# Performance work log

Hardware: AMD Instinct MI355X
Metric: run time of the kernel (lower is better)

## Reference

```python
import jax, jax.numpy as jnp
import numpy as np

N = 100000   # num_nodes
R = 8        # num_relations
D = 64       # hidden_dim
E = 3200000  # num_edges


def setup_inputs() -> dict:
    key = jax.random.key(0)
    ks = jax.random.split(key, 10)
    s = 1.0 / np.sqrt(D)
    return {
        "x": jnp.arange(N, dtype=jnp.int64),
        "edge_index": jax.random.randint(ks[0], (2, E), 0, N, dtype=jnp.int64),
        "edge_type": jax.random.randint(ks[1], (E,), 0, R, dtype=jnp.int64),
        "emb": jax.random.normal(ks[2], (N, D), dtype=jnp.float32),
        "W1": jax.random.normal(ks[3], (R, D, D), dtype=jnp.float32) * s,
        "root1": jax.random.normal(ks[4], (D, D), dtype=jnp.float32) * s,
        "b1": jnp.zeros((D,), dtype=jnp.float32),
        "W2": jax.random.normal(ks[5], (R, D, D), dtype=jnp.float32) * s,
        "root2": jax.random.normal(ks[6], (D, D), dtype=jnp.float32) * s,
        "b2": jnp.zeros((D,), dtype=jnp.float32),
    }


def rgcn_conv(h, W, root, b, src, dst, etype):
    # per-edge gather of source features: [E, D]
    msgs = h[src]
    # composite segment id: (dst, relation) -> dst * R + relation
    seg = dst * R + etype
    sums = jax.ops.segment_sum(msgs, seg, num_segments=N * R)          # [N*R, D]
    cnt = jax.ops.segment_sum(jnp.ones((msgs.shape[0],), h.dtype), seg,
                              num_segments=N * R)                       # [N*R]
    mean = sums / jnp.maximum(cnt, 1.0)[:, None]                        # per-relation mean aggr
    mean = mean.reshape(N, R, D)
    # relation-specific transform + root weight + bias
    return jnp.einsum('nrd,rde->ne', mean, W) + h @ root + b


def reference(x, edge_index, edge_type, emb, W1, root1, b1, W2, root2, b2):
    src, dst = edge_index[0], edge_index[1]
    h = emb[x]                                   # embedding lookup
    h = rgcn_conv(h, W1, root1, b1, src, dst, edge_type)
    h = jax.nn.relu(h)                           # dropout = identity (eval mode)
    h = rgcn_conv(h, W2, root2, b2, src, dst, edge_type)
    return h
```

## Files before the change

kernel.cpp:

```cpp
#include <hip/hip_runtime.h>

#define N_NODES 100000
#define R_REL   8
#define D_DIM   64
#define E_EDGES 3200000
#define NSEG    (N_NODES * R_REL)
#define NB      782
#define SEG_PER_BKT 1024
#define BKT_CAP 4800
#define P1_BLOCKS 625
#define P1_CHUNK  5120

typedef __attribute__((ext_vector_type(8))) short short8;
typedef __attribute__((ext_vector_type(4))) float f32x4;

__device__ __forceinline__ unsigned short f2bf(float f) {
    unsigned u = __float_as_uint(f);
    u += 0x7fffu + ((u >> 16) & 1u);
    return (unsigned short)(u >> 16);
}

__device__ __forceinline__ int epack(int s, int d, int r) {
    return (s << 10) | ((d & 127) << 3) | r;
}

__global__ void __launch_bounds__(256)
cvt_kernel(const float* __restrict__ in, unsigned short* __restrict__ outb) {
    size_t base = ((size_t)blockIdx.x * 256 + threadIdx.x) * 8;
    float4 v0 = *(const float4*)(in + base);
    float4 v1 = *(const float4*)(in + base + 4);
    uint4 o;
    o.x = f2bf(v0.x) | ((unsigned)f2bf(v0.y) << 16);
    o.y = f2bf(v0.z) | ((unsigned)f2bf(v0.w) << 16);
    o.z = f2bf(v1.x) | ((unsigned)f2bf(v1.y) << 16);
    o.w = f2bf(v1.z) | ((unsigned)f2bf(v1.w) << 16);
    *(uint4*)(outb + base) = o;
}

__global__ void init_cursor_kernel(int* __restrict__ bkt_cursor) {
    int t = blockIdx.x * 256 + threadIdx.x;
    if (t <= NB) bkt_cursor[t] = t * BKT_CAP;
}

__global__ void __launch_bounds__(256)
p1_scatter_kernel(const int* __restrict__ src, const int* __restrict__ dst,
                  const int* __restrict__ et, int* __restrict__ bkt_cursor,
                  int* __restrict__ packed) {
    __shared__ int hist[NB];
    __shared__ int cur[NB];
    int t = threadIdx.x;
    for (int i = t; i < NB; i += 256) hist[i] = 0;
    __syncthreads();
    int base = blockIdx.x * P1_CHUNK;
    for (int i = t * 4; i < P1_CHUNK; i += 1024) {
        int4 d4 = *(const int4*)(dst + base + i);
        atomicAdd(&hist[d4.x >> 7], 1);
        atomicAdd(&hist[d4.y >> 7], 1);
        atomicAdd(&hist[d4.z >> 7], 1);
        atomicAdd(&hist[d4.w >> 7], 1);
    }
    __syncthreads();
    for (int i = t; i < NB; i += 256) {
        int c = hist[i];
        cur[i] = c ? atomicAdd(&bkt_cursor[i], c) : 0;
    }
    __syncthreads();
    for (int i = t * 4; i < P1_CHUNK; i += 1024) {
        int4 s4 = *(const int4*)(src + base + i);
        int4 d4 = *(const int4*)(dst + base + i);
        int4 t4 = *(const int4*)(et  + base + i);
        int p0 = atomicAdd(&cur[d4.x >> 7], 1); packed[p0] = epack(s4.x, d4.x, t4.x);
        int p1 = atomicAdd(&cur[d4.y >> 7], 1); packed[p1] = epack(s4.y, d4.y, t4.y);
        int p2 = atomicAdd(&cur[d4.z >> 7], 1); packed[p2] = epack(s4.z, d4.z, t4.z);
        int p3 = atomicAdd(&cur[d4.w >> 7], 1); packed[p3] = epack(s4.w, d4.w, t4.w);
    }
}

__global__ void __launch_bounds__(256)
p2_sort_kernel(const int* __restrict__ packed, const int* __restrict__ bkt_cursor,
               int* __restrict__ starts, int* __restrict__ ends, int* __restrict__ esrc) {
    __shared__ int spk[BKT_CAP];
    __shared__ int shist[SEG_PER_BKT];
    __shared__ int scur[SEG_PER_BKT];
    __shared__ int stmp[256];
    int b = blockIdx.x;
    int t = threadIdx.x;
    int ebase = b * BKT_CAP;
    int ecnt  = bkt_cursor[b] - ebase;
    int segbase = b * SEG_PER_BKT;
    int nseg = NSEG - segbase; if (nseg > SEG_PER_BKT) nseg = SEG_PER_BKT;
#pragma unroll
    for (int i = 0; i < 4; ++i) shist[t + i * 256] = 0;
    __syncthreads();
    for (int i = t; i < ecnt; i += 256) {
        int p = packed[ebase + i];
        spk[i] = p;
        atomicAdd(&shist[p & 1023], 1);
    }
    __syncthreads();
    int loc[4], s = 0;
    int b4 = t * 4;
#pragma unroll
    for (int i = 0; i < 4; ++i) { loc[i] = shist[b4 + i]; s += loc[i]; }
    stmp[t] = s;
    __syncthreads();
    for (int off = 1; off < 256; off <<= 1) {
        int x = (t >= off) ? stmp[t - off] : 0;
        __syncthreads();
        stmp[t] += x;
        __syncthreads();
    }
    int run = (t == 0) ? 0 : stmp[t - 1];
#pragma unroll
    for (int i = 0; i < 4; ++i) {
        shist[b4 + i] = run; scur[b4 + i] = run;
        run += loc[i];
    }
    __syncthreads();
    for (int i = t; i < nseg; i += 256)
        starts[segbase + i] = ebase + shist[i];
    for (int i = t; i < ecnt; i += 256) {
        int p = spk[i];
        int r = atomicAdd(&scur[p & 1023], 1);
        esrc[ebase + r] = p >> 10;
    }
    __syncthreads();
    for (int i = t; i < nseg; i += 256)
        ends[segbase + i] = ebase + scur[i];
}

__global__ void wprep_kernel(const float* __restrict__ W, const float* __restrict__ root,
                             unsigned short* __restrict__ wbuf) {
    int r = blockIdx.x;
    const float* src = (r < 8) ? (W + (size_t)r * 4096) : root;
    __shared__ float t[64][65];
    int a = threadIdx.x >> 2, c = threadIdx.x & 3;
#pragma unroll
    for (int i = 0; i < 4; ++i) {
        float4 v = *(const float4*)(src + a * 64 + c * 16 + i * 4);
        t[a][c * 16 + i * 4 + 0] = v.x;
        t[a][c * 16 + i * 4 + 1] = v.y;
        t[a][c * 16 + i * 4 + 2] = v.z;
        t[a][c * 16 + i * 4 + 3] = v.w;
    }
    __syncthreads();
    unsigned short* outrow = wbuf + (size_t)r * 4096 + a * 64;
#pragma unroll
    for (int i = 0; i < 4; ++i) {
        int k0 = c * 16 + i * 4;
        ushort4 o;
        o.x = f2bf(t[k0 + 0][a]); o.y = f2bf(t[k0 + 1][a]);
        o.z = f2bf(t[k0 + 2][a]); o.w = f2bf(t[k0 + 3][a]);
        *(ushort4*)(outrow + k0) = o;
    }
}

__global__ void __launch_bounds__(512, 6)
fused_kernel(const unsigned short* __restrict__ hb, const int* __restrict__ esrc,
             const int* __restrict__ starts, const int* __restrict__ ends,
             const unsigned short* __restrict__ wbuf, const float* __restrict__ bias,
             void* __restrict__ out, int mode) {
    __shared__ unsigned short As[8][32][72];
    __shared__ int sS[256], sE[256];
    __shared__ int pool;
    int tid = threadIdx.x;
    int ml  = tid & 15;
    int n0  = blockIdx.x * 32;
    int sblk = n0 * R_REL;

    if (tid < 256) sS[tid] = starts[sblk + tid];
    else           sE[tid - 256] = ends[sblk + tid - 256];
    if (tid == 0) pool = 0;
    __syncthreads();

#define ACC4(P0,P1,P2,P3, RW, M)                                         \
    do {                                                                 \
        _Pragma("unroll")                                                \
        for (int i = 0; i < 4; ++i) if (i < (M)) {                       \
            P0 += __uint_as_float(RW[i].x << 16);                        \
            P1 += __uint_as_float(RW[i].x & 0xffff0000u);                \
            P2 += __uint_as_float(RW[i].y << 16);                        \
            P3 += __uint_as_float(RW[i].y & 0xffff0000u);                \
        }                                                                \
    } while (0)

#define LOAD4(RW, B, E)                                                  \
    do {                                                                 \
        _Pragma("unroll")                                                \
        for (int i = 0; i < 4; ++i) {                                    \
            int ee = (B) + i; ee = (ee < (E)) ? ee : ((E) - 1);          \
            int sid = esrc[ee];                                          \
            RW[i] = *(const uint2*)(hb + (size_t)sid * D_DIM + ml * 4);  \
        }                                                                \
    } while (0)

    while (true) {
        int s2 = 0;
        if (ml == 0) s2 = atomicAdd(&pool, 2);
        s2 = __shfl(s2, 0, 16);
        if (s2 >= 256) break;
        int b0 = sS[s2],     e0 = sE[s2];
        int b1 = sS[s2 + 1], e1 = sE[s2 + 1];
        int c0 = e0 - b0, c1 = e1 - b1;
        float p0 = 0.f, p1 = 0.f, p2 = 0.f, p3 = 0.f;
        float q0 = 0.f, q1 = 0.f, q2 = 0.f, q3 = 0.f;
        while (b0 < e0 || b1 < e1) {
            int m0 = e0 - b0; m0 = (m0 > 4) ? 4 : m0;
            int m1 = e1 - b1; m1 = (m1 > 4) ? 4 : m1;
            uint2 rA[4], rB[4];
            if (m0 > 0) LOAD4(rA, b0, e0);
            if (m1 > 0) LOAD4(rB, b1, e1);
            if (m0 > 0) { ACC4(p0, p1, p2, p3, rA, m0); b0 += m0; }
            if (m1 > 0) { ACC4(q0, q1, q2, q3, rB, m1); b1 += m1; }
        }
        int nl = s2 >> 3, r = s2 & 7;
        {
            float inv = __builtin_amdgcn_rcpf(fmaxf((float)c0, 1.0f));
            ushort4 o;
            o.x = f2bf(p0 * inv); o.y = f2bf(p1 * inv);
            o.z = f2bf(p2 * inv); o.w = f2bf(p3 * inv);
            *(ushort4*)(&As[r][nl][ml * 4]) = o;
        }
        {
            float inv = __builtin_amdgcn_rcpf(fmaxf((float)c1, 1.0f));
            ushort4 o;
            o.x = f2bf(q0 * inv); o.y = f2bf(q1 * inv);
            o.z = f2bf(q2 * inv); o.w = f2bf(q3 * inv);
            *(ushort4*)(&As[r + 1][nl][ml * 4]) = o;
        }
    }
#undef ACC4
#undef LOAD4

    int w  = tid >> 6;
    int kg = (tid >> 4) & 3;
    int h  = w & 1;
    int q  = w >> 1;

    const unsigned short* rp = hb + (size_t)(n0 + h * 16 + ml) * D_DIM + kg * 8;
    short8 RA0 = *(const short8*)(rp);
    short8 RA1 = *(const short8*)(rp + 32);

    __syncthreads();

    f32x4 acc = {0, 0, 0, 0};
#pragma unroll 1
    for (int p = 0; p < 8; ++p) {
        short8 A0 = *(const short8*)(&As[p][h * 16 + ml][kg * 8]);
        short8 A1 = *(const short8*)(&As[p][h * 16 + ml][kg * 8 + 32]);
        const unsigned short* bp = wbuf + (size_t)p * 4096 + (q * 16 + ml) * 64 + kg * 8;
        short8 B0 = *(const short8*)(bp);
        short8 B1 = *(const short8*)(bp + 32);
        acc = __builtin_amdgcn_mfma_f32_16x16x32_bf16(A0, B0, acc, 0, 0, 0);
        acc = __builtin_amdgcn_mfma_f32_16x16x32_bf16(A1, B1, acc, 0, 0, 0);
    }
    {
        const unsigned short* bp = wbuf + (size_t)8 * 4096 + (q * 16 + ml) * 64 + kg * 8;
        short8 B0 = *(const short8*)(bp);
        short8 B1 = *(const short8*)(bp + 32);
        acc = __builtin_amdgcn_mfma_f32_16x16x32_bf16(RA0, B0, acc, 0, 0, 0);
        acc = __builtin_amdgcn_mfma_f32_16x16x32_bf16(RA1, B1, acc, 0, 0, 0);
    }

    float bv = bias[q * 16 + ml];
#pragma unroll
    for (int rg = 0; rg < 4; ++rg) {
        int node = n0 + h * 16 + kg * 4 + rg;
        float v = acc[rg] + bv;
        if (mode) {
            v = fmaxf(v, 0.f);
            ((unsigned short*)out)[(size_t)node * D_DIM + q * 16 + ml] = f2bf(v);
        } else {
            ((float*)out)[(size_t)node * D_DIM + q * 16 + ml] = v;
        }
    }
}


extern "C" void kernel_launch(void* const* d_in, const int* in_sizes, int n_in,
                              void* d_out, int out_size, void* d_ws, size_t ws_size,
                              hipStream_t stream) {
    const int*   ei    = (const int*)d_in[1];
    const int*   src   = ei;
    const int*   dst   = ei + E_EDGES;
    const int*   et    = (const int*)d_in[2];
    const float* emb   = (const float*)d_in[3];
    const float* W1    = (const float*)d_in[4];
    const float* root1 = (const float*)d_in[5];
    const float* b1    = (const float*)d_in[6];
    const float* W2    = (const float*)d_in[7];
    const float* root2 = (const float*)d_in[8];
    const float* b2    = (const float*)d_in[9];
    float*       out   = (float*)d_out;

    unsigned short* embb   = (unsigned short*)d_ws;
    unsigned short* h1b    = embb + (size_t)N_NODES * D_DIM;
    unsigned short* wbuf1  = h1b + (size_t)N_NODES * D_DIM;
    unsigned short* wbuf2  = wbuf1 + 9 * 4096;
    int*            starts = (int*)(wbuf2 + 9 * 4096);
    int*            ends   = starts + NSEG;
    int*            packed = ends + NSEG;
    int*            esrc   = packed + (size_t)NB * BKT_CAP;
    int*            bkt_cursor = esrc + (size_t)NB * BKT_CAP;

    init_cursor_kernel<<<4, 256, 0, stream>>>(bkt_cursor);
    p1_scatter_kernel <<<P1_BLOCKS, 256, 0, stream>>>(src, dst, et, bkt_cursor, packed);
    p2_sort_kernel    <<<NB, 256, 0, stream>>>(packed, bkt_cursor, starts, ends, esrc);

    wprep_kernel<<<9, 256, 0, stream>>>(W1, root1, wbuf1);
    wprep_kernel<<<9, 256, 0, stream>>>(W2, root2, wbuf2);
    cvt_kernel<<<(N_NODES * D_DIM) / 2048, 256, 0, stream>>>(emb, embb);

    const int blocks = N_NODES / 32;

    fused_kernel<<<blocks, 512, 0, stream>>>(embb, esrc, starts, ends, wbuf1, b1, h1b, 1);
    fused_kernel<<<blocks, 512, 0, stream>>>(h1b, esrc, starts, ends, wbuf2, b2, out, 0);
}
```

Baseline: 459.8 us.

## Balance edge aggregation across waves by edge ranges and merge prep kernels

The aggregation phase of the fused kernel now stages the block's source-index list in LDS and splits the block's edge range evenly across the 8 waves. Each wave walks consecutive segments, with one lane per feature reading 2-byte values. Segments that cross a wave boundary are merged through shared-memory atomics in a fix-up pass. This replaces dynamic per-segment assignment and is meant to remove load imbalance from varying segment sizes. It adds LDS staging, a zeroing pass, an extra barrier, and smaller per-lane loads, and it assumes at most 1536 edges per block. The two weight-prep launches and the embedding conversion are also combined into a single kernel.

```diff
diff --git a/kernel.cpp b/kernel.cpp
--- a/kernel.cpp
+++ b/kernel.cpp
@@ -10,6 +10,7 @@
 #define BKT_CAP 4800
 #define P1_BLOCKS 625
 #define P1_CHUNK  5120
+#define ESRC_CAP 1536
 
 typedef __attribute__((ext_vector_type(8))) short short8;
 typedef __attribute__((ext_vector_type(4))) float f32x4;
@@ -22,19 +23,6 @@
 
 __device__ __forceinline__ int epack(int s, int d, int r) {
     return (s << 10) | ((d & 127) << 3) | r;
-}
-
-__global__ void __launch_bounds__(256)
-cvt_kernel(const float* __restrict__ in, unsigned short* __restrict__ outb) {
-    size_t base = ((size_t)blockIdx.x * 256 + threadIdx.x) * 8;
-    float4 v0 = *(const float4*)(in + base);
-    float4 v1 = *(const float4*)(in + base + 4);
-    uint4 o;
-    o.x = f2bf(v0.x) | ((unsigned)f2bf(v0.y) << 16);
-    o.y = f2bf(v0.z) | ((unsigned)f2bf(v0.w) << 16);
-    o.z = f2bf(v1.x) | ((unsigned)f2bf(v1.y) << 16);
-    o.w = f2bf(v1.z) | ((unsigned)f2bf(v1.w) << 16);
-    *(uint4*)(outb + base) = o;
 }
 
 __global__ void init_cursor_kernel(int* __restrict__ bkt_cursor) {
@@ -129,29 +117,49 @@
         ends[segbase + i] = ebase + scur[i];
 }
 
-__global__ void wprep_kernel(const float* __restrict__ W, const float* __restrict__ root,
-                             unsigned short* __restrict__ wbuf) {
-    int r = blockIdx.x;
-    const float* src = (r < 8) ? (W + (size_t)r * 4096) : root;
-    __shared__ float t[64][65];
-    int a = threadIdx.x >> 2, c = threadIdx.x & 3;
-#pragma unroll
-    for (int i = 0; i < 4; ++i) {
-        float4 v = *(const float4*)(src + a * 64 + c * 16 + i * 4);
-        t[a][c * 16 + i * 4 + 0] = v.x;
-        t[a][c * 16 + i * 4 + 1] = v.y;
-        t[a][c * 16 + i * 4 + 2] = v.z;
-        t[a][c * 16 + i * 4 + 3] = v.w;
-    }
-    __syncthreads();
-    unsigned short* outrow = wbuf + (size_t)r * 4096 + a * 64;
-#pragma unroll
-    for (int i = 0; i < 4; ++i) {
-        int k0 = c * 16 + i * 4;
-        ushort4 o;
-        o.x = f2bf(t[k0 + 0][a]); o.y = f2bf(t[k0 + 1][a]);
-        o.z = f2bf(t[k0 + 2][a]); o.w = f2bf(t[k0 + 3][a]);
-        *(ushort4*)(outrow + k0) = o;
+__global__ void __launch_bounds__(256)
+prep_kernel(const float* __restrict__ W1, const float* __restrict__ root1,
+            const float* __restrict__ W2, const float* __restrict__ root2,
+            const float* __restrict__ emb,
+            unsigned short* __restrict__ wbuf1, unsigned short* __restrict__ wbuf2,
+            unsigned short* __restrict__ embb) {
+    int b = blockIdx.x;
+    if (b < 18) {
+        int r = (b < 9) ? b : b - 9;
+        const float* W    = (b < 9) ? W1 : W2;
+        const float* root = (b < 9) ? root1 : root2;
+        unsigned short* wbuf = (b < 9) ? wbuf1 : wbuf2;
+        const float* src = (r < 8) ? (W + (size_t)r * 4096) : root;
+        __shared__ float t[64][65];
+        int a = threadIdx.x >> 2, c = threadIdx.x & 3;
+#pragma unroll
+        for (int i = 0; i < 4; ++i) {
+            float4 v = *(const float4*)(src + a * 64 + c * 16 + i * 4);
+            t[a][c * 16 + i * 4 + 0] = v.x;
+            t[a][c * 16 + i * 4 + 1] = v.y;
+            t[a][c * 16 + i * 4 + 2] = v.z;
+            t[a][c * 16 + i * 4 + 3] = v.w;
+        }
+        __syncthreads();
+        unsigned short* outrow = wbuf + (size_t)r * 4096 + a * 64;
+#pragma unroll
+        for (int i = 0; i < 4; ++i) {
+            int k0 = c * 16 + i * 4;
+            ushort4 o;
+            o.x = f2bf(t[k0 + 0][a]); o.y = f2bf(t[k0 + 1][a]);
+            o.z = f2bf(t[k0 + 2][a]); o.w = f2bf(t[k0 + 3][a]);
+            *(ushort4*)(outrow + k0) = o;
+        }
+    } else {
+        size_t base = ((size_t)(b - 18) * 256 + threadIdx.x) * 8;
+        float4 v0 = *(const float4*)(emb + base);
+        float4 v1 = *(const float4*)(emb + base + 4);
+        uint4 o;
+        o.x = f2bf(v0.x) | ((unsigned)f2bf(v0.y) << 16);
+        o.y = f2bf(v0.z) | ((unsigned)f2bf(v0.w) << 16);
+        o.z = f2bf(v1.x) | ((unsigned)f2bf(v1.y) << 16);
+        o.w = f2bf(v1.z) | ((unsigned)f2bf(v1.w) << 16);
+        *(uint4*)(embb + base) = o;
     }
 }
 
@@ -161,81 +169,120 @@
              const unsigned short* __restrict__ wbuf, const float* __restrict__ bias,
              void* __restrict__ out, int mode) {
     __shared__ unsigned short As[8][32][72];
-    __shared__ int sS[256], sE[256];
-    __shared__ int pool;
-    int tid = threadIdx.x;
-    int ml  = tid & 15;
-    int n0  = blockIdx.x * 32;
+    __shared__ int esrc_lds[ESRC_CAP];
+    __shared__ int sSl[256];
+    __shared__ int sEl[256];
+    __shared__ float bnd[8][64];
+    __shared__ int bseg[8];
+    __shared__ int bflag[8];
+
+    int tid  = threadIdx.x;
+    int wid  = tid >> 6;
+    int lane = tid & 63;
+    int n0   = blockIdx.x * 32;
     int sblk = n0 * R_REL;
 
-    if (tid < 256) sS[tid] = starts[sblk + tid];
-    else           sE[tid - 256] = ends[sblk + tid - 256];
-    if (tid == 0) pool = 0;
-    __syncthreads();
-
-#define ACC4(P0,P1,P2,P3, RW, M)                                         \
-    do {                                                                 \
-        _Pragma("unroll")                                                \
-        for (int i = 0; i < 4; ++i) if (i < (M)) {                       \
-            P0 += __uint_as_float(RW[i].x << 16);                        \
-            P1 += __uint_as_float(RW[i].x & 0xffff0000u);                \
-            P2 += __uint_as_float(RW[i].y << 16);                        \
-            P3 += __uint_as_float(RW[i].y & 0xffff0000u);                \
-        }                                                                \
+    int E0g = starts[sblk];
+    int L   = ends[sblk + 255] - E0g;
+
+    {
+        int* a32 = (int*)&As[0][0][0];
+        for (int i = tid; i < 8 * 32 * 36; i += 512) a32[i] = 0;
+        ((float*)bnd)[tid] = 0.f;
+        if (tid < 8) bflag[tid] = 0;
+    }
+    if (tid < 256) sSl[tid] = starts[sblk + tid] - E0g;
+    else           sEl[tid - 256] = ends[sblk + tid - 256] - E0g;
+    for (int i = tid; i < L; i += 512) esrc_lds[i] = esrc[E0g + i];
+    __syncthreads();
+
+    int ck = ((L + 63) >> 6) << 3;
+    int ws = wid * ck;
+    int we = ws + ck; if (we > L) we = L;
+
+    if (ws < L) {
+        int lo = 0, hi = 255;
+        while (lo < hi) { int mid = (lo + hi) >> 1; if (sEl[mid] > ws) hi = mid; else lo = mid + 1; }
+        int seg = lo;
+        int segS = sSl[seg], segE = sEl[seg];
+        bool leftB = (segS < ws);
+        if (leftB && lane == 0) { bseg[wid] = seg; bflag[wid] = 1; }
+        bool firstF = true;
+        float acc = 0.f;
+        const char* hb8 = (const char*)hb;
+        unsigned laneoff = (unsigned)(lane * 2);
+
+#define PREPLOAD(OFF, DATA, CB)                                       \
+    do {                                                              \
+        _Pragma("unroll")                                             \
+        for (int i_ = 0; i_ < 8; ++i_) {                              \
+            int e_ = (CB) + i_; e_ = (e_ < L) ? e_ : (L - 1);         \
+            OFF[i_] = (unsigned)esrc_lds[e_] * 128u + laneoff;        \
+        }                                                             \
+        _Pragma("unroll")                                             \
+        for (int i_ = 0; i_ < 8; ++i_)                                \
+            DATA[i_] = *(const unsigned short*)(hb8 + OFF[i_]);       \
     } while (0)
 
-#define LOAD4(RW, B, E)                                                  \
-    do {                                                                 \
-        _Pragma("unroll")                                                \
-        for (int i = 0; i < 4; ++i) {                                    \
-            int ee = (B) + i; ee = (ee < (E)) ? ee : ((E) - 1);          \
-            int sid = esrc[ee];                                          \
-            RW[i] = *(const uint2*)(hb + (size_t)sid * D_DIM + ml * 4);  \
-        }                                                                \
+#define FLUSHSEG()                                                    \
+    do {                                                              \
+        if (firstF && leftB) {                                        \
+            atomicAdd(&bnd[wid][lane], acc);                          \
+        } else {                                                      \
+            float m_ = acc * __builtin_amdgcn_rcpf(                   \
+                fmaxf((float)(segE - segS), 1.0f));                   \
+            As[seg & 7][seg >> 3][lane] = f2bf(m_);                   \
+        }                                                             \
+        firstF = false; acc = 0.f;                                    \
+        ++seg; segS = segE; segE = sEl[seg];                          \
     } while (0)
 
-    while (true) {
-        int s2 = 0;
-        if (ml == 0) s2 = atomicAdd(&pool, 2);
-        s2 = __shfl(s2, 0, 16);
-        if (s2 >= 256) break;
-        int b0 = sS[s2],     e0 = sE[s2];
-        int b1 = sS[s2 + 1], e1 = sE[s2 + 1];
-        int c0 = e0 - b0, c1 = e1 - b1;
-        float p0 = 0.f, p1 = 0.f, p2 = 0.f, p3 = 0.f;
-        float q0 = 0.f, q1 = 0.f, q2 = 0.f, q3 = 0.f;
-        while (b0 < e0 || b1 < e1) {
-            int m0 = e0 - b0; m0 = (m0 > 4) ? 4 : m0;
-            int m1 = e1 - b1; m1 = (m1 > 4) ? 4 : m1;
-            uint2 rA[4], rB[4];
-            if (m0 > 0) LOAD4(rA, b0, e0);
-            if (m1 > 0) LOAD4(rB, b1, e1);
-            if (m0 > 0) { ACC4(p0, p1, p2, p3, rA, m0); b0 += m0; }
-            if (m1 > 0) { ACC4(q0, q1, q2, q3, rB, m1); b1 += m1; }
-        }
-        int nl = s2 >> 3, r = s2 & 7;
-        {
-            float inv = __builtin_amdgcn_rcpf(fmaxf((float)c0, 1.0f));
-            ushort4 o;
-            o.x = f2bf(p0 * inv); o.y = f2bf(p1 * inv);
-            o.z = f2bf(p2 * inv); o.w = f2bf(p3 * inv);
-            *(ushort4*)(&As[r][nl][ml * 4]) = o;
-        }
-        {
-            float inv = __builtin_amdgcn_rcpf(fmaxf((float)c1, 1.0f));
-            ushort4 o;
-            o.x = f2bf(q0 * inv); o.y = f2bf(q1 * inv);
-            o.z = f2bf(q2 * inv); o.w = f2bf(q3 * inv);
-            *(ushort4*)(&As[r + 1][nl][ml * 4]) = o;
-        }
-    }
-#undef ACC4
-#undef LOAD4
-
-    int w  = tid >> 6;
+#define CONSUME(DATA, CB)                                             \
+    do {                                                              \
+        _Pragma("unroll")                                             \
+        for (int i_ = 0; i_ < 8; ++i_) {                              \
+            int e_ = (CB) + i_;                                       \
+            if (e_ >= we) break;                                      \
+            while (e_ >= segE) FLUSHSEG();                            \
+            acc += __uint_as_float(DATA[i_] << 16);                   \
+        }                                                             \
+    } while (0)
+
+        unsigned offA[8], offB[8], dataA[8], dataB[8];
+        PREPLOAD(offA, dataA, ws);
+        int cb = ws;
+        while (true) {
+            if (cb + 8 < we) PREPLOAD(offB, dataB, cb + 8);
+            CONSUME(dataA, cb);
+            cb += 8;
+            if (cb >= we) break;
+            if (cb + 8 < we) PREPLOAD(offA, dataA, cb + 8);
+            CONSUME(dataB, cb);
+            cb += 8;
+            if (cb >= we) break;
+        }
+        if (segS < we) {
+            if (we == segE) {
+                if (firstF && leftB) atomicAdd(&bnd[wid][lane], acc);
+                else {
+                    float m_ = acc * __builtin_amdgcn_rcpf(
+                        fmaxf((float)(segE - segS), 1.0f));
+                    As[seg & 7][seg >> 3][lane] = f2bf(m_);
+                }
+            } else {
+                if (firstF && leftB) atomicAdd(&bnd[wid][lane], acc);
+                else atomicAdd(&bnd[wid + 1][lane], acc);
+            }
+        }
+#undef PREPLOAD
+#undef FLUSHSEG
+#undef CONSUME
+    }
+
+    int ml = tid & 15;
     int kg = (tid >> 4) & 3;
-    int h  = w & 1;
-    int q  = w >> 1;
+    int h  = wid & 1;
+    int q  = wid >> 1;
 
     const unsigned short* rp = hb + (size_t)(n0 + h * 16 + ml) * D_DIM + kg * 8;
     short8 RA0 = *(const short8*)(rp);
@@ -243,7 +290,15 @@
 
     __syncthreads();
 
-    f32x4 acc = {0, 0, 0, 0};
+    if (wid >= 1 && bflag[wid]) {
+        int s_ = bseg[wid];
+        float c_ = (float)(sEl[s_] - sSl[s_]);
+        float m_ = bnd[wid][lane] * __builtin_amdgcn_rcpf(fmaxf(c_, 1.0f));
+        As[s_ & 7][s_ >> 3][lane] = f2bf(m_);
+    }
+    __syncthreads();
+
+    f32x4 acc4 = {0, 0, 0, 0};
 #pragma unroll 1
     for (int p = 0; p < 8; ++p) {
         short8 A0 = *(const short8*)(&As[p][h * 16 + ml][kg * 8]);
@@ -251,22 +306,22 @@
         const unsigned short* bp = wbuf + (size_t)p * 4096 + (q * 16 + ml) * 64 + kg * 8;
         short8 B0 = *(const short8*)(bp);
         short8 B1 = *(const short8*)(bp + 32);
-        acc = __builtin_amdgcn_mfma_f32_16x16x32_bf16(A0, B0, acc, 0, 0, 0);
-        acc = __builtin_amdgcn_mfma_f32_16x16x32_bf16(A1, B1, acc, 0, 0, 0);
+        acc4 = __builtin_amdgcn_mfma_f32_16x16x32_bf16(A0, B0, acc4, 0, 0, 0);
+        acc4 = __builtin_amdgcn_mfma_f32_16x16x32_bf16(A1, B1, acc4, 0, 0, 0);
     }
     {
         const unsigned short* bp = wbuf + (size_t)8 * 4096 + (q * 16 + ml) * 64 + kg * 8;
         short8 B0 = *(const short8*)(bp);
         short8 B1 = *(const short8*)(bp + 32);
-        acc = __builtin_amdgcn_mfma_f32_16x16x32_bf16(RA0, B0, acc, 0, 0, 0);
-        acc = __builtin_amdgcn_mfma_f32_16x16x32_bf16(RA1, B1, acc, 0, 0, 0);
+        acc4 = __builtin_amdgcn_mfma_f32_16x16x32_bf16(RA0, B0, acc4, 0, 0, 0);
+        acc4 = __builtin_amdgcn_mfma_f32_16x16x32_bf16(RA1, B1, acc4, 0, 0, 0);
     }
 
     float bv = bias[q * 16 + ml];
 #pragma unroll
     for (int rg = 0; rg < 4; ++rg) {
         int node = n0 + h * 16 + kg * 4 + rg;
-        float v = acc[rg] + bv;
+        float v = acc4[rg] + bv;
         if (mode) {
             v = fmaxf(v, 0.f);
             ((unsigned short*)out)[(size_t)node * D_DIM + q * 16 + ml] = f2bf(v);
@@ -307,9 +362,8 @@
     p1_scatter_kernel <<<P1_BLOCKS, 256, 0, stream>>>(src, dst, et, bkt_cursor, packed);
     p2_sort_kernel    <<<NB, 256, 0, stream>>>(packed, bkt_cursor, starts, ends, esrc);
 
-    wprep_kernel<<<9, 256, 0, stream>>>(W1, root1, wbuf1);
-    wprep_kernel<<<9, 256, 0, stream>>>(W2, root2, wbuf2);
-    cvt_kernel<<<(N_NODES * D_DIM) / 2048, 256, 0, stream>>>(emb, embb);
+    prep_kernel<<<18 + (N_NODES * D_DIM) / 2048, 256, 0, stream>>>(
+        W1, root1, W2, root2, emb, wbuf1, wbuf2, embb);
 
     const int blocks = N_NODES / 32;
 
```

Result: slower. 526.1 us (+14.4%).
